# Optimization experiments

Hardware: AMD Instinct MI355X
Metric: run time of the kernel (lower is better)

## Reference

```python
import jax, jax.numpy as jnp
import numpy as np

N = 65536          # pixels
F = 224            # spectral bands (num_features)
P = 6              # num_endmembers
H = 256            # hidden_dim


def setup_inputs() -> dict:
    key = jax.random.key(0)
    ks = jax.random.split(key, 8)
    s = lambda fan_in: 1.0 / np.sqrt(fan_in)
    return {
        "abundance_matrix": jax.random.normal(ks[0], (N, P), jnp.float32),
        "Y": jax.random.normal(ks[1], (N, F), jnp.float32),
        "W1": jax.random.normal(ks[2], (F, H), jnp.float32) * s(F),
        "b1": jnp.zeros((H,), jnp.float32),
        "W2": jax.random.normal(ks[3], (H, H), jnp.float32) * s(H),
        "b2": jnp.zeros((H,), jnp.float32),
        "W3": jax.random.normal(ks[4], (H, F), jnp.float32) * s(H),
        "b3": jnp.zeros((F,), jnp.float32),
    }


def reference(abundance_matrix, Y, W1, b1, W2, b2, W3, b3):
    # MLP is pointwise over pixels, so apply once to all pixels [N,F] -> [N,F]
    h = jax.nn.relu(Y @ W1 + b1)
    h = jax.nn.relu(h @ W2 + b2)
    logits = h @ W3 + b3                      # [N, F]

    cls = jnp.argmax(abundance_matrix, axis=-1)          # [N]
    masks = cls[None, :] == jnp.arange(P)[:, None]       # [P, N]

    # Masked per-class softmax over the pixel axis (per feature column).
    neg = jnp.finfo(logits.dtype).min
    masked_logits = jnp.where(masks[:, :, None], logits[None], neg)  # [P, N, F]
    w = jax.nn.softmax(masked_logits, axis=1)                        # [P, N, F]
    w = w * masks[:, :, None]                                        # exact zeros off-class

    M = jnp.einsum('pnf,nf->pf', w, Y)                   # [P, F] endmembers
    counts = masks.sum(axis=1)                           # [P]
    M = jnp.where((counts > 0)[:, None], M, jnp.zeros_like(M))

    Y_hat = abundance_matrix @ M                         # [N, F]
    return Y_hat
```

## Files before the change

kernel.cpp:

```cpp
#include <hip/hip_runtime.h>
#include <stdint.h>

typedef short s16x8 __attribute__((ext_vector_type(8)));
typedef short s16x4 __attribute__((ext_vector_type(4)));
typedef float f32x4 __attribute__((ext_vector_type(4)));

#define NPIX 65536
#define FEAT 224
#define PEND 6
#define HID  256

__device__ __forceinline__ unsigned short f2bf(float x) {
  unsigned u = __float_as_uint(x);
  return (unsigned short)((u + 0x7FFFu + ((u >> 16) & 1u)) >> 16);
}
__device__ __forceinline__ float bf2f(unsigned short b) {
  return __uint_as_float(((unsigned)b) << 16);
}
__device__ __forceinline__ void glds16(const void* g, void* l) {
  __builtin_amdgcn_global_load_lds(
      (const __attribute__((address_space(1))) unsigned int*)g,
      (__attribute__((address_space(3))) unsigned int*)l, 16, 0, 0);
}

__global__ void cvtW_all(const float* __restrict__ W1, const float* __restrict__ W2,
                         const float* __restrict__ W3,
                         unsigned short* __restrict__ W1t, unsigned short* __restrict__ W2t,
                         unsigned short* __restrict__ W3t) {
  int i = blockIdx.x * 256 + threadIdx.x;
  if (i < 57344) {
    int n = i / 224, k = i - n * 224;
    W1t[i] = f2bf(W1[k * 256 + n]);
  } else if (i < 122880) {
    int i2 = i - 57344;
    int n = i2 >> 8, k = i2 & 255;
    W2t[i2] = f2bf(W2[k * 256 + n]);
  } else if (i < 188416) {
    int i3 = i - 122880;
    int n = i3 >> 8, k = i3 & 255;
    W3t[i3] = (n < FEAT) ? f2bf(W3[k * FEAT + n]) : (unsigned short)0;
  }
}

__global__ __launch_bounds__(256, 2)
void fused_mlp(const float* __restrict__ Y,
               const unsigned short* __restrict__ W1t,
               const unsigned short* __restrict__ W2t,
               const unsigned short* __restrict__ W3t,
               const float* __restrict__ b1, const float* __restrict__ b2,
               const float* __restrict__ b3, const float* __restrict__ ab,
               float* __restrict__ gsum, float* __restrict__ gsumY) {
  constexpr int HPAD = 264;
  constexpr int APAD = 36;
  __shared__ __align__(16) unsigned short hS[64 * HPAD];
  __shared__ __align__(16) unsigned short As[64 * APAD];
  __shared__ __align__(16) unsigned short Bs[256 * 32];
  __shared__ __align__(16) float redE[PEND * FEAT];
  __shared__ __align__(16) float redY[PEND * FEAT];
  const int tid = threadIdx.x;
  const int wid = tid >> 6;
  const int lane = tid & 63;
  const int wm = wid >> 1, wn = wid & 1;
  const int mrow = lane & 15, quad = lane >> 4;
  const long row0 = (long)blockIdx.x * 64;

  const int brow = lane >> 2;
  const int bk8 = (lane & 3) * 8;
  unsigned short* BsW = Bs + (wid * 64) * 32;
  const int arow = tid >> 2, aqtr = tid & 3;

  f32x4 acc[2][8];

#pragma unroll
  for (int i = 0; i < 2; i++)
#pragma unroll
    for (int j = 0; j < 8; j++) acc[i][j] = {0.f, 0.f, 0.f, 0.f};

  for (int p = 0; p < 7; p++) {
    const int k0 = p * 32;
    {
      const float* src = Y + (row0 + arow) * FEAT + k0 + aqtr * 8;
      float4 v0 = *(const float4*)src;
      float4 v1 = *(const float4*)(src + 4);
      s16x4 lo = {(short)f2bf(v0.x), (short)f2bf(v0.y), (short)f2bf(v0.z), (short)f2bf(v0.w)};
      s16x4 hi = {(short)f2bf(v1.x), (short)f2bf(v1.y), (short)f2bf(v1.z), (short)f2bf(v1.w)};
      *(s16x4*)(As + arow * APAD + aqtr * 8) = lo;
      *(s16x4*)(As + arow * APAD + aqtr * 8 + 4) = hi;
    }
#pragma unroll
    for (int c = 0; c < 4; c++)
      glds16(W1t + (size_t)(wid * 64 + c * 16 + brow) * FEAT + k0 + bk8, BsW + c * 16 * 32);
    __syncthreads();
    s16x8 af[2], bfv[8];
#pragma unroll
    for (int i = 0; i < 2; i++) {
      const unsigned short* pa = As + (wm * 32 + i * 16 + mrow) * APAD + quad * 8;
      s16x4 lo = *(const s16x4*)pa, hi = *(const s16x4*)(pa + 4);
      af[i] = __builtin_shufflevector(lo, hi, 0, 1, 2, 3, 4, 5, 6, 7);
    }
#pragma unroll
    for (int j = 0; j < 8; j++)
      bfv[j] = *(const s16x8*)(Bs + (wn * 128 + j * 16 + mrow) * 32 + quad * 8);
#pragma unroll
    for (int i = 0; i < 2; i++)
#pragma unroll
      for (int j = 0; j < 8; j++)
        acc[i][j] = __builtin_amdgcn_mfma_f32_16x16x32_bf16(af[i], bfv[j], acc[i][j], 0, 0, 0);
    __syncthreads();
  }
#pragma unroll
  for (int j = 0; j < 8; j++) {
    int col = wn * 128 + j * 16 + mrow;
    float bb = b1[col];
#pragma unroll
    for (int i = 0; i < 2; i++) {
      int r0 = wm * 32 + i * 16 + quad * 4;
#pragma unroll
      for (int r = 0; r < 4; r++)
        hS[(r0 + r) * HPAD + col] = f2bf(fmaxf(acc[i][j][r] + bb, 0.f));
    }
  }
  __syncthreads();

#pragma unroll
  for (int i = 0; i < 2; i++)
#pragma unroll
    for (int j = 0; j < 8; j++) acc[i][j] = {0.f, 0.f, 0.f, 0.f};
  for (int p = 0; p < 8; p++) {
    const int k0 = p * 32;
#pragma unroll
    for (int c = 0; c < 4; c++)
      glds16(W2t + (size_t)(wid * 64 + c * 16 + brow) * HID + k0 + bk8, BsW + c * 16 * 32);
    __syncthreads();
    s16x8 af[2], bfv[8];
#pragma unroll
    for (int i = 0; i < 2; i++)
      af[i] = *(const s16x8*)(hS + (wm * 32 + i * 16 + mrow) * HPAD + k0 + quad * 8);
#pragma unroll
    for (int j = 0; j < 8; j++)
      bfv[j] = *(const s16x8*)(Bs + (wn * 128 + j * 16 + mrow) * 32 + quad * 8);
#pragma unroll
    for (int i = 0; i < 2; i++)
#pragma unroll
      for (int j = 0; j < 8; j++)
        acc[i][j] = __builtin_amdgcn_mfma_f32_16x16x32_bf16(af[i], bfv[j], acc[i][j], 0, 0, 0);
    __syncthreads();
  }
#pragma unroll
  for (int j = 0; j < 8; j++) {
    int col = wn * 128 + j * 16 + mrow;
    float bb = b2[col];
#pragma unroll
    for (int i = 0; i < 2; i++) {
      int r0 = wm * 32 + i * 16 + quad * 4;
#pragma unroll
      for (int r = 0; r < 4; r++)
        hS[(r0 + r) * HPAD + col] = f2bf(fmaxf(acc[i][j][r] + bb, 0.f));
    }
  }
  __syncthreads();

#pragma unroll
  for (int i = 0; i < 2; i++)
#pragma unroll
    for (int j = 0; j < 8; j++) acc[i][j] = {0.f, 0.f, 0.f, 0.f};
  for (int p = 0; p < 8; p++) {
    const int k0 = p * 32;
#pragma unroll
    for (int c = 0; c < 4; c++)
      glds16(W3t + (size_t)(wid * 64 + c * 16 + brow) * HID + k0 + bk8, BsW + c * 16 * 32);
    __syncthreads();
    s16x8 af[2], bfv[8];
#pragma unroll
    for (int i = 0; i < 2; i++)
      af[i] = *(const s16x8*)(hS + (wm * 32 + i * 16 + mrow) * HPAD + k0 + quad * 8);
#pragma unroll
    for (int j = 0; j < 8; j++)
      bfv[j] = *(const s16x8*)(Bs + (wn * 128 + j * 16 + mrow) * 32 + quad * 8);
#pragma unroll
    for (int i = 0; i < 2; i++)
#pragma unroll
      for (int j = 0; j < 8; j++)
        acc[i][j] = __builtin_amdgcn_mfma_f32_16x16x32_bf16(af[i], bfv[j], acc[i][j], 0, 0, 0);
    __syncthreads();
  }
#pragma unroll
  for (int j = 0; j < 8; j++) {
    int col = wn * 128 + j * 16 + mrow;
    if (col < FEAT) {
      float bb = b3[col];
#pragma unroll
      for (int i = 0; i < 2; i++) {
        int r0 = wm * 32 + i * 16 + quad * 4;
#pragma unroll
        for (int r = 0; r < 4; r++)
          hS[(r0 + r) * HPAD + col] = f2bf(__expf(acc[i][j][r] + bb));
      }
    }
  }
  __syncthreads();

  const bool act = lane < 56;
  const int f0 = lane * 4;
  float accE[PEND][4], accY[PEND][4];
#pragma unroll
  for (int p = 0; p < PEND; p++)
#pragma unroll
    for (int i = 0; i < 4; i++) { accE[p][i] = 0.f; accY[p][i] = 0.f; }

  for (int r = wid; r < 64; r += 4) {
    const float* a = ab + (row0 + r) * PEND;
    float best = a[0]; int c = 0;
#pragma unroll
    for (int p = 1; p < PEND; p++) { float v = a[p]; if (v > best) { best = v; c = p; } }
    c = __builtin_amdgcn_readfirstlane(c);
    if (act) {
      ushort4 e4 = *(const ushort4*)(hS + r * HPAD + f0);
      float4 y4 = *(const float4*)(Y + (row0 + r) * FEAT + f0);
      float e[4] = {bf2f(e4.x), bf2f(e4.y), bf2f(e4.z), bf2f(e4.w)};
      float ey[4] = {e[0] * y4.x, e[1] * y4.y, e[2] * y4.z, e[3] * y4.w};
#define RK_CASE(P)                                                               \
      case P:                                                                    \
        _Pragma("unroll")                                                        \
        for (int i = 0; i < 4; i++) { accE[P][i] += e[i]; accY[P][i] += ey[i]; } \
        break;
      switch (c) {
        RK_CASE(0) RK_CASE(1) RK_CASE(2) RK_CASE(3) RK_CASE(4) RK_CASE(5)
      }
#undef RK_CASE
    }
  }

  for (int w = 0; w < 4; w++) {
    if (wid == w && act) {
#pragma unroll
      for (int p = 0; p < PEND; p++) {
        float4* pe = (float4*)(redE + p * FEAT + f0);
        float4* py = (float4*)(redY + p * FEAT + f0);
        float4 ve = {accE[p][0], accE[p][1], accE[p][2], accE[p][3]};
        float4 vy = {accY[p][0], accY[p][1], accY[p][2], accY[p][3]};
        if (w == 0) { *pe = ve; *py = vy; }
        else {
          float4 oe = *pe, oy = *py;
          oe.x += ve.x; oe.y += ve.y; oe.z += ve.z; oe.w += ve.w;
          oy.x += vy.x; oy.y += vy.y; oy.z += vy.z; oy.w += vy.w;
          *pe = oe; *py = oy;
        }
      }
    }
    __syncthreads();
  }

  for (int i = tid; i < PEND * FEAT; i += 256) {
    atomicAdd(&gsum[i], redE[i]);
    atomicAdd(&gsumY[i], redY[i]);
  }
}

__global__ __launch_bounds__(256)
void yhat(const float* __restrict__ ab, const float* __restrict__ gsum,
          const float* __restrict__ gsumY, float* __restrict__ out) {
  constexpr int ROWS = 64;
  __shared__ float Ms[PEND * FEAT];
  __shared__ float aS[ROWS * PEND];
  const int tid = threadIdx.x;
  for (int i = tid; i < PEND * FEAT; i += 256) {
    float s = gsum[i];
    Ms[i] = (s > 0.f) ? gsumY[i] / s : 0.f;
  }
  const long n0 = (long)blockIdx.x * ROWS;
  for (int i = tid; i < ROWS * PEND; i += 256) aS[i] = ab[n0 * PEND + i];
  __syncthreads();

  const int wid = tid >> 6;
  const int lane = tid & 63;
  if (lane >= 56) return;
  const int f0 = lane * 4;
  float4 Mr[PEND];
#pragma unroll
  for (int p = 0; p < PEND; p++) Mr[p] = *(const float4*)(Ms + p * FEAT + f0);

  for (int r = wid; r < ROWS; r += 4) {
    float a[PEND];
#pragma unroll
    for (int p = 0; p < PEND; p++) a[p] = aS[r * PEND + p];
    float4 o = {0.f, 0.f, 0.f, 0.f};
#pragma unroll
    for (int p = 0; p < PEND; p++) {
      o.x += a[p] * Mr[p].x; o.y += a[p] * Mr[p].y;
      o.z += a[p] * Mr[p].z; o.w += a[p] * Mr[p].w;
    }
    *(float4*)(out + (n0 + r) * FEAT + f0) = o;
  }
}

extern "C" void kernel_launch(void* const* d_in, const int* in_sizes, int n_in,
                              void* d_out, int out_size, void* d_ws, size_t ws_size,
                              hipStream_t stream) {
  const float* ab = (const float*)d_in[0];
  const float* Y  = (const float*)d_in[1];
  const float* W1 = (const float*)d_in[2];
  const float* b1 = (const float*)d_in[3];
  const float* W2 = (const float*)d_in[4];
  const float* b2 = (const float*)d_in[5];
  const float* W3 = (const float*)d_in[6];
  const float* b3 = (const float*)d_in[7];
  float* out = (float*)d_out;

  char* ws = (char*)d_ws;
  const size_t oW1t  = 0;
  const size_t oW2t  = 114688;
  const size_t oW3t  = 245760;
  const size_t osum  = 376832;

  unsigned short* W1t = (unsigned short*)(ws + oW1t);
  unsigned short* W2t = (unsigned short*)(ws + oW2t);
  unsigned short* W3t = (unsigned short*)(ws + oW3t);
  float* gsum  = (float*)(ws + osum);
  float* gsumY = (float*)(ws + osum + 5376);

  hipMemsetAsync(ws + osum, 0, 2 * 5376, stream);
  cvtW_all<<<736, 256, 0, stream>>>(W1, W2, W3, W1t, W2t, W3t);
  fused_mlp<<<1024, 256, 0, stream>>>(Y, W1t, W2t, W3t, b1, b2, b3, ab, gsum, gsumY);
  yhat<<<1024, 256, 0, stream>>>(ab, gsum, gsumY, out);
}
```

Baseline: 216.9 us.

## Double-buffer weight tiles across all three GEMM stages, swizzle hidden LDS

Weight tiles are now double-buffered and staged one step ahead, including across layer boundaries, so global-to-LDS loads overlap MFMA work and each k-step needs one barrier instead of two. The Y input tile is prefetched into registers and aliased into the hidden buffer. The hidden buffer uses an XOR swizzle instead of padding, which lowers LDS use. Argmax is computed once per row into shared memory, and the memset is folded into the weight-convert kernel to save a launch. In exchange the code carries more register pressure and more complex buffer-aliasing invariants.

```diff
diff --git a/kernel.cpp b/kernel.cpp
--- a/kernel.cpp
+++ b/kernel.cpp
@@ -26,7 +26,7 @@
 __global__ void cvtW_all(const float* __restrict__ W1, const float* __restrict__ W2,
                          const float* __restrict__ W3,
                          unsigned short* __restrict__ W1t, unsigned short* __restrict__ W2t,
-                         unsigned short* __restrict__ W3t) {
+                         unsigned short* __restrict__ W3t, float* __restrict__ gz) {
   int i = blockIdx.x * 256 + threadIdx.x;
   if (i < 57344) {
     int n = i / 224, k = i - n * 224;
@@ -39,6 +39,8 @@
     int i3 = i - 122880;
     int n = i3 >> 8, k = i3 & 255;
     W3t[i3] = (n < FEAT) ? f2bf(W3[k * FEAT + n]) : (unsigned short)0;
+  } else if (i < 191104) {
+    gz[i - 188416] = 0.f;
   }
 }
 
@@ -50,138 +52,149 @@
                const float* __restrict__ b1, const float* __restrict__ b2,
                const float* __restrict__ b3, const float* __restrict__ ab,
                float* __restrict__ gsum, float* __restrict__ gsumY) {
-  constexpr int HPAD = 264;
-  constexpr int APAD = 36;
-  __shared__ __align__(16) unsigned short hS[64 * HPAD];
-  __shared__ __align__(16) unsigned short As[64 * APAD];
-  __shared__ __align__(16) unsigned short Bs[256 * 32];
-  __shared__ __align__(16) float redE[PEND * FEAT];
-  __shared__ __align__(16) float redY[PEND * FEAT];
+  __shared__ __align__(16) unsigned short hS[64 * 256];
+  __shared__ __align__(16) unsigned short Bs[2][8192];
+  unsigned short* AsB = hS;
+  float* redE = (float*)&Bs[0][0];
+  float* redY = redE + PEND * FEAT;
+  unsigned short* clsS = (unsigned short*)(redY + PEND * FEAT);
+
   const int tid = threadIdx.x;
-  const int wid = tid >> 6;
-  const int lane = tid & 63;
+  const int wid = tid >> 6, lane = tid & 63;
   const int wm = wid >> 1, wn = wid & 1;
   const int mrow = lane & 15, quad = lane >> 4;
+  const int brow = lane >> 2, bk8 = (lane & 3) * 8;
+  const int arow = tid >> 2, aqtr = tid & 3;
   const long row0 = (long)blockIdx.x * 64;
 
-  const int brow = lane >> 2;
-  const int bk8 = (lane & 3) * 8;
-  unsigned short* BsW = Bs + (wid * 64) * 32;
-  const int arow = tid >> 2, aqtr = tid & 3;
-
   f32x4 acc[2][8];
-
-#pragma unroll
-  for (int i = 0; i < 2; i++)
-#pragma unroll
-    for (int j = 0; j < 8; j++) acc[i][j] = {0.f, 0.f, 0.f, 0.f};
-
+  float4 pv0, pv1;
+
+#define STAGE_W(s) do {                                                     \
+    const unsigned short* Wp_; int ld_, k0_;                                \
+    if ((s) < 7)       { Wp_ = W1t; ld_ = 224; k0_ = (s) * 32; }            \
+    else if ((s) < 15) { Wp_ = W2t; ld_ = 256; k0_ = ((s) - 7) * 32; }      \
+    else               { Wp_ = W3t; ld_ = 256; k0_ = ((s) - 15) * 32; }     \
+    unsigned short* dst_ = &Bs[(s) & 1][wid * 2048];                        \
+    _Pragma("unroll")                                                       \
+    for (int c_ = 0; c_ < 4; c_++)                                          \
+      glds16(Wp_ + (wid * 64 + c_ * 16 + brow) * ld_ + k0_ + bk8,           \
+             dst_ + c_ * 512);                                              \
+  } while (0)
+
+#define LOADA(p) do {                                                       \
+    const float* s_ = Y + (row0 + arow) * FEAT + (p) * 32 + aqtr * 8;       \
+    pv0 = *(const float4*)s_; pv1 = *(const float4*)(s_ + 4);               \
+  } while (0)
+
+#define WRITEA(p) do {                                                      \
+    unsigned short* d_ = AsB + ((p) & 1) * 2304 + arow * 36 + aqtr * 8;     \
+    s16x4 lo_ = {(short)f2bf(pv0.x), (short)f2bf(pv0.y),                    \
+                 (short)f2bf(pv0.z), (short)f2bf(pv0.w)};                   \
+    s16x4 hi_ = {(short)f2bf(pv1.x), (short)f2bf(pv1.y),                    \
+                 (short)f2bf(pv1.z), (short)f2bf(pv1.w)};                   \
+    *(s16x4*)d_ = lo_; *(s16x4*)(d_ + 4) = hi_;                             \
+  } while (0)
+
+#define LOAD_B(buf)                                                         \
+    _Pragma("unroll")                                                       \
+    for (int j = 0; j < 8; j++)                                             \
+      bfv[j] = *(const s16x8*)(&Bs[buf][(wn * 128 + j * 16 + mrow) * 32 + quad * 8]);
+
+#define MFMA_ALL()                                                          \
+    _Pragma("unroll")                                                       \
+    for (int i = 0; i < 2; i++)                                             \
+      _Pragma("unroll")                                                     \
+      for (int j = 0; j < 8; j++)                                           \
+        acc[i][j] = __builtin_amdgcn_mfma_f32_16x16x32_bf16(af[i], bfv[j], acc[i][j], 0, 0, 0);
+
+#define ZERO_ACC()                                                          \
+    _Pragma("unroll")                                                       \
+    for (int i = 0; i < 2; i++)                                             \
+      _Pragma("unroll")                                                     \
+      for (int j = 0; j < 8; j++) acc[i][j] = {0.f, 0.f, 0.f, 0.f};
+
+  ZERO_ACC();
+  LOADA(0); STAGE_W(0); WRITEA(0);
+  __syncthreads();
   for (int p = 0; p < 7; p++) {
-    const int k0 = p * 32;
-    {
-      const float* src = Y + (row0 + arow) * FEAT + k0 + aqtr * 8;
-      float4 v0 = *(const float4*)src;
-      float4 v1 = *(const float4*)(src + 4);
-      s16x4 lo = {(short)f2bf(v0.x), (short)f2bf(v0.y), (short)f2bf(v0.z), (short)f2bf(v0.w)};
-      s16x4 hi = {(short)f2bf(v1.x), (short)f2bf(v1.y), (short)f2bf(v1.z), (short)f2bf(v1.w)};
-      *(s16x4*)(As + arow * APAD + aqtr * 8) = lo;
-      *(s16x4*)(As + arow * APAD + aqtr * 8 + 4) = hi;
-    }
-#pragma unroll
-    for (int c = 0; c < 4; c++)
-      glds16(W1t + (size_t)(wid * 64 + c * 16 + brow) * FEAT + k0 + bk8, BsW + c * 16 * 32);
-    __syncthreads();
+    if (p < 6) { LOADA(p + 1); STAGE_W(p + 1); }
+    else       { STAGE_W(7); }
     s16x8 af[2], bfv[8];
-#pragma unroll
-    for (int i = 0; i < 2; i++) {
-      const unsigned short* pa = As + (wm * 32 + i * 16 + mrow) * APAD + quad * 8;
+    const unsigned short* Ab = AsB + (p & 1) * 2304;
+#pragma unroll
+    for (int i = 0; i < 2; i++) {
+      const unsigned short* pa = Ab + (wm * 32 + i * 16 + mrow) * 36 + quad * 8;
       s16x4 lo = *(const s16x4*)pa, hi = *(const s16x4*)(pa + 4);
       af[i] = __builtin_shufflevector(lo, hi, 0, 1, 2, 3, 4, 5, 6, 7);
     }
-#pragma unroll
-    for (int j = 0; j < 8; j++)
-      bfv[j] = *(const s16x8*)(Bs + (wn * 128 + j * 16 + mrow) * 32 + quad * 8);
-#pragma unroll
-    for (int i = 0; i < 2; i++)
-#pragma unroll
-      for (int j = 0; j < 8; j++)
-        acc[i][j] = __builtin_amdgcn_mfma_f32_16x16x32_bf16(af[i], bfv[j], acc[i][j], 0, 0, 0);
+    LOAD_B(p & 1);
+    MFMA_ALL();
+    if (p < 6) WRITEA(p + 1);
     __syncthreads();
   }
 #pragma unroll
   for (int j = 0; j < 8; j++) {
     int col = wn * 128 + j * 16 + mrow;
     float bb = b1[col];
+    int cs = col >> 3, c7 = col & 7;
 #pragma unroll
     for (int i = 0; i < 2; i++) {
       int r0 = wm * 32 + i * 16 + quad * 4;
 #pragma unroll
-      for (int r = 0; r < 4; r++)
-        hS[(r0 + r) * HPAD + col] = f2bf(fmaxf(acc[i][j][r] + bb, 0.f));
-    }
-  }
-  __syncthreads();
-
-#pragma unroll
-  for (int i = 0; i < 2; i++)
-#pragma unroll
-    for (int j = 0; j < 8; j++) acc[i][j] = {0.f, 0.f, 0.f, 0.f};
+      for (int r = 0; r < 4; r++) {
+        int row = r0 + r;
+        hS[row * 256 + ((cs ^ (row & 7)) << 3) + c7] = f2bf(fmaxf(acc[i][j][r] + bb, 0.f));
+      }
+    }
+  }
+  __syncthreads();
+
+  ZERO_ACC();
   for (int p = 0; p < 8; p++) {
-    const int k0 = p * 32;
-#pragma unroll
-    for (int c = 0; c < 4; c++)
-      glds16(W2t + (size_t)(wid * 64 + c * 16 + brow) * HID + k0 + bk8, BsW + c * 16 * 32);
-    __syncthreads();
+    STAGE_W(p < 7 ? 8 + p : 15);
+    const int k0 = p * 32, buf = (p + 1) & 1;
     s16x8 af[2], bfv[8];
 #pragma unroll
-    for (int i = 0; i < 2; i++)
-      af[i] = *(const s16x8*)(hS + (wm * 32 + i * 16 + mrow) * HPAD + k0 + quad * 8);
-#pragma unroll
-    for (int j = 0; j < 8; j++)
-      bfv[j] = *(const s16x8*)(Bs + (wn * 128 + j * 16 + mrow) * 32 + quad * 8);
-#pragma unroll
-    for (int i = 0; i < 2; i++)
-#pragma unroll
-      for (int j = 0; j < 8; j++)
-        acc[i][j] = __builtin_amdgcn_mfma_f32_16x16x32_bf16(af[i], bfv[j], acc[i][j], 0, 0, 0);
+    for (int i = 0; i < 2; i++) {
+      int R = wm * 32 + i * 16 + mrow;
+      int ch = (k0 >> 3) + quad;
+      af[i] = *(const s16x8*)(hS + R * 256 + ((ch ^ (R & 7)) << 3));
+    }
+    LOAD_B(buf);
+    MFMA_ALL();
     __syncthreads();
   }
 #pragma unroll
   for (int j = 0; j < 8; j++) {
     int col = wn * 128 + j * 16 + mrow;
     float bb = b2[col];
+    int cs = col >> 3, c7 = col & 7;
 #pragma unroll
     for (int i = 0; i < 2; i++) {
       int r0 = wm * 32 + i * 16 + quad * 4;
 #pragma unroll
-      for (int r = 0; r < 4; r++)
-        hS[(r0 + r) * HPAD + col] = f2bf(fmaxf(acc[i][j][r] + bb, 0.f));
-    }
-  }
-  __syncthreads();
-
-#pragma unroll
-  for (int i = 0; i < 2; i++)
-#pragma unroll
-    for (int j = 0; j < 8; j++) acc[i][j] = {0.f, 0.f, 0.f, 0.f};
+      for (int r = 0; r < 4; r++) {
+        int row = r0 + r;
+        hS[row * 256 + ((cs ^ (row & 7)) << 3) + c7] = f2bf(fmaxf(acc[i][j][r] + bb, 0.f));
+      }
+    }
+  }
+  __syncthreads();
+
+  ZERO_ACC();
   for (int p = 0; p < 8; p++) {
-    const int k0 = p * 32;
-#pragma unroll
-    for (int c = 0; c < 4; c++)
-      glds16(W3t + (size_t)(wid * 64 + c * 16 + brow) * HID + k0 + bk8, BsW + c * 16 * 32);
-    __syncthreads();
+    if (p < 7) STAGE_W(16 + p);
+    const int k0 = p * 32, buf = (p + 1) & 1;
     s16x8 af[2], bfv[8];
 #pragma unroll
-    for (int i = 0; i < 2; i++)
-      af[i] = *(const s16x8*)(hS + (wm * 32 + i * 16 + mrow) * HPAD + k0 + quad * 8);
-#pragma unroll
-    for (int j = 0; j < 8; j++)
-      bfv[j] = *(const s16x8*)(Bs + (wn * 128 + j * 16 + mrow) * 32 + quad * 8);
-#pragma unroll
-    for (int i = 0; i < 2; i++)
-#pragma unroll
-      for (int j = 0; j < 8; j++)
-        acc[i][j] = __builtin_amdgcn_mfma_f32_16x16x32_bf16(af[i], bfv[j], acc[i][j], 0, 0, 0);
+    for (int i = 0; i < 2; i++) {
+      int R = wm * 32 + i * 16 + mrow;
+      int ch = (k0 >> 3) + quad;
+      af[i] = *(const s16x8*)(hS + R * 256 + ((ch ^ (R & 7)) << 3));
+    }
+    LOAD_B(buf);
+    MFMA_ALL();
     __syncthreads();
   }
 #pragma unroll
@@ -189,14 +202,24 @@
     int col = wn * 128 + j * 16 + mrow;
     if (col < FEAT) {
       float bb = b3[col];
+      int cs = col >> 3, c7 = col & 7;
 #pragma unroll
       for (int i = 0; i < 2; i++) {
         int r0 = wm * 32 + i * 16 + quad * 4;
 #pragma unroll
-        for (int r = 0; r < 4; r++)
-          hS[(r0 + r) * HPAD + col] = f2bf(__expf(acc[i][j][r] + bb));
-      }
-    }
+        for (int r = 0; r < 4; r++) {
+          int row = r0 + r;
+          hS[row * 256 + ((cs ^ (row & 7)) << 3) + c7] = f2bf(__expf(acc[i][j][r] + bb));
+        }
+      }
+    }
+  }
+  if (tid < 64) {
+    const float* a = ab + (row0 + tid) * PEND;
+    float best = a[0]; int c = 0;
+#pragma unroll
+    for (int p = 1; p < PEND; p++) { float v = a[p]; if (v > best) { best = v; c = p; } }
+    clsS[tid] = (unsigned short)c;
   }
   __syncthreads();
 
@@ -208,14 +231,12 @@
 #pragma unroll
     for (int i = 0; i < 4; i++) { accE[p][i] = 0.f; accY[p][i] = 0.f; }
 
+#pragma unroll 4
   for (int r = wid; r < 64; r += 4) {
-    const float* a = ab + (row0 + r) * PEND;
-    float best = a[0]; int c = 0;
-#pragma unroll
-    for (int p = 1; p < PEND; p++) { float v = a[p]; if (v > best) { best = v; c = p; } }
-    c = __builtin_amdgcn_readfirstlane(c);
+    int c = __builtin_amdgcn_readfirstlane((int)clsS[r]);
     if (act) {
-      ushort4 e4 = *(const ushort4*)(hS + r * HPAD + f0);
+      const unsigned short* pe = hS + r * 256 + (((f0 >> 3) ^ (r & 7)) << 3) + (f0 & 7);
+      ushort4 e4 = *(const ushort4*)pe;
       float4 y4 = *(const float4*)(Y + (row0 + r) * FEAT + f0);
       float e[4] = {bf2f(e4.x), bf2f(e4.y), bf2f(e4.z), bf2f(e4.w)};
       float ey[4] = {e[0] * y4.x, e[1] * y4.y, e[2] * y4.z, e[3] * y4.w};
@@ -255,6 +276,12 @@
     atomicAdd(&gsum[i], redE[i]);
     atomicAdd(&gsumY[i], redY[i]);
   }
+#undef STAGE_W
+#undef LOADA
+#undef WRITEA
+#undef LOAD_B
+#undef MFMA_ALL
+#undef ZERO_ACC
 }
 
 __global__ __launch_bounds__(256)
@@ -319,8 +346,7 @@
   float* gsum  = (float*)(ws + osum);
   float* gsumY = (float*)(ws + osum + 5376);
 
-  hipMemsetAsync(ws + osum, 0, 2 * 5376, stream);
-  cvtW_all<<<736, 256, 0, stream>>>(W1, W2, W3, W1t, W2t, W3t);
+  cvtW_all<<<747, 256, 0, stream>>>(W1, W2, W3, W1t, W2t, W3t, gsum);
   fused_mlp<<<1024, 256, 0, stream>>>(Y, W1t, W2t, W3t, b1, b2, b3, ab, gsum, gsumY);
   yhat<<<1024, 256, 0, stream>>>(ab, gsum, gsumY, out);
 }
```

Result: faster. 203.9 us (-6.0%).
